# Optimization experiments

Hardware: AMD Instinct MI355X
Metric: run time of the kernel (lower is better)

The kernel has to match this reference:

```python
import jax, jax.numpy as jnp
import numpy as np

N0 = 260000  # all sampled nodes (hop-2 sources)
N1 = 60000   # hop-1 targets / hop-2 sources
N2 = 10000   # final batch targets
E1 = 1500000
E2 = 250000
DIN, DH, DOUT = 128, 256, 128


def sage_conv(x_src, x_tgt, src, dst, n_tgt, Wl, b, Wr):
    # mean aggregation of source features over incoming edges per target,
    # then lin_l(agg) + lin_r(x_tgt)  (PyG SAGEConv default, lin_r has no bias)
    msg = x_src[src]                                             # [E, d]
    agg = jax.ops.segment_sum(msg, dst, num_segments=n_tgt)      # [n_tgt, d]
    cnt = jax.ops.segment_sum(jnp.ones((src.shape[0], 1), x_src.dtype), dst,
                              num_segments=n_tgt)                # [n_tgt, 1]
    agg = agg / jnp.maximum(cnt, 1.0)
    return agg @ Wl + b + x_tgt @ Wr


def setup_inputs() -> dict:
    key = jax.random.key(0)
    ks = jax.random.split(key, 10)
    s = 1.0 / np.sqrt(DIN)
    s2 = 1.0 / np.sqrt(DH)
    return {
        "x": jax.random.normal(ks[0], (N0, DIN), dtype=jnp.float32),
        "W1l": jax.random.normal(ks[1], (DIN, DH), dtype=jnp.float32) * s,
        "b1": jnp.zeros((DH,), dtype=jnp.float32),
        "W1r": jax.random.normal(ks[2], (DIN, DH), dtype=jnp.float32) * s,
        "W2l": jax.random.normal(ks[3], (DH, DOUT), dtype=jnp.float32) * s2,
        "b2": jnp.zeros((DOUT,), dtype=jnp.float32),
        "W2r": jax.random.normal(ks[4], (DH, DOUT), dtype=jnp.float32) * s2,
        "src1": jax.random.randint(ks[5], (E1,), 0, N0, dtype=jnp.int32),
        "dst1": jax.random.randint(ks[6], (E1,), 0, N1, dtype=jnp.int32),
        "src2": jax.random.randint(ks[7], (E2,), 0, N1, dtype=jnp.int32),
        "dst2": jax.random.randint(ks[8], (E2,), 0, N2, dtype=jnp.int32),
    }


def reference(x, W1l, b1, W1r, W2l, b2, W2r, src1, dst1, src2, dst2):
    h = sage_conv(x, x[:N1], src1, dst1, N1, W1l, b1, W1r)  # [N1, DH]
    h = jax.nn.relu(h)
    out = sage_conv(h, h[:N2], src2, dst2, N2, W2l, b2, W2r)  # [N2, DOUT]
    return out
```

## Files before the change

kernel.cpp:

```cpp
#include <hip/hip_runtime.h>
#include <hip/hip_bf16.h>

#define N0 260000
#define N1 60000
#define N2 10000
#define E1 1500000
#define E2 250000
#define DIN 128
#define DH 256
#define DOUT 128
#define CAP 80

typedef __attribute__((ext_vector_type(8))) short bf16x8;
typedef __attribute__((ext_vector_type(4))) float f32x4;
typedef __attribute__((ext_vector_type(2))) float f32x2;
typedef __attribute__((ext_vector_type(4))) unsigned uivec4;

#define MFMA16(a, b, c) __builtin_amdgcn_mfma_f32_16x16x32_bf16(a, b, c, 0, 0, 0)

__device__ inline float blo(unsigned u) { return __uint_as_float(u << 16); }
__device__ inline float bhi(unsigned u) { return __uint_as_float(u & 0xFFFF0000u); }
__device__ inline unsigned short f2b(float f) {
    unsigned u = __float_as_uint(f);
    return (unsigned short)((u + 0x7FFFu + ((u >> 16) & 1u)) >> 16);
}

__device__ inline unsigned pack4_fp8(float4 f) {
    int w = 0;
    w = __builtin_amdgcn_cvt_pk_fp8_f32(f.x, f.y, w, false);
    w = __builtin_amdgcn_cvt_pk_fp8_f32(f.z, f.w, w, true);
    return (unsigned)w;
}
__device__ inline void acc8h(float* acc, uint2 v) {
    f32x2 a0 = __builtin_amdgcn_cvt_pk_f32_fp8((int)v.x, false);
    f32x2 a1 = __builtin_amdgcn_cvt_pk_f32_fp8((int)v.x, true);
    f32x2 a2 = __builtin_amdgcn_cvt_pk_f32_fp8((int)v.y, false);
    f32x2 a3 = __builtin_amdgcn_cvt_pk_f32_fp8((int)v.y, true);
    acc[0] += a0.x; acc[1] += a0.y; acc[2] += a1.x; acc[3] += a1.y;
    acc[4] += a2.x; acc[5] += a2.y; acc[6] += a3.x; acc[7] += a3.y;
}

#define BB_C1 256
#define BB_C2 64
#define BUILD2_BLOCKS (8 * BB_C2)
#define P1ROWS (N1 / 8)
#define P2ROWS (N2 / 8)
#define CONVX_BLOCKS 8125
#define CONVW_BLOCKS 512
#define CONV_TOTAL (CONVX_BLOCKS + CONVW_BLOCKS)
#define PERIOD 40
#define NPERIODS 256
#define INTERLEAVED (PERIOD * NPERIODS)
#define PREP_TAIL (CONV_TOTAL - 32 * NPERIODS)
#define PREP_BLOCKS (INTERLEAVED + PREP_TAIL)
__global__ __launch_bounds__(256) void prep9(const float* __restrict__ x, unsigned char* __restrict__ xb,
                                             const float* __restrict__ W1l, const float* __restrict__ W1r,
                                             const float* __restrict__ W2l, const float* __restrict__ W2r,
                                             unsigned short* __restrict__ W1lt, unsigned short* __restrict__ W1rt,
                                             unsigned short* __restrict__ W2lt, unsigned short* __restrict__ W2rt,
                                             const int* __restrict__ src1, const int* __restrict__ dst1,
                                             int* __restrict__ cnt1, int* __restrict__ csr1,
                                             int use_xb) {
    int b = blockIdx.x;
    int t = threadIdx.x;
    int conv_idx;
    if (b < INTERLEAVED) {
        int p = b / PERIOD, r = b % PERIOD;
        if (r < 8) {
            if (b == 0 && t < 16 && use_xb) {
                uint2 z; z.x = 0u; z.y = 0u;
                reinterpret_cast<uint2*>(xb + (size_t)N0 * DIN)[t] = z;
            }
            int lo = r * P1ROWS, hi = lo + P1ROWS;
            const int4* d4 = reinterpret_cast<const int4*>(dst1);
            const int4* s4 = reinterpret_cast<const int4*>(src1);
            for (int i = p * 256 + t; i < E1 / 4; i += BB_C1 * 256) {
                int4 d = d4[i];
                int4 s = s4[i];
                if (d.x >= lo && d.x < hi) { int q = atomicAdd(&cnt1[d.x], 1); if (q < CAP) csr1[d.x * CAP + q] = s.x; }
                if (d.y >= lo && d.y < hi) { int q = atomicAdd(&cnt1[d.y], 1); if (q < CAP) csr1[d.y * CAP + q] = s.y; }
                if (d.z >= lo && d.z < hi) { int q = atomicAdd(&cnt1[d.z], 1); if (q < CAP) csr1[d.z * CAP + q] = s.z; }
                if (d.w >= lo && d.w < hi) { int q = atomicAdd(&cnt1[d.w], 1); if (q < CAP) csr1[d.w * CAP + q] = s.w; }
            }
            return;
        }
        conv_idx = p * 32 + (r - 8);
    } else {
        conv_idx = 32 * NPERIODS + (b - INTERLEAVED);
    }
    if (conv_idx < CONVX_BLOCKS) {
        if (!use_xb) return;
        size_t i = (size_t)conv_idx * 256 + t;
        const float4* xf = reinterpret_cast<const float4*>(x) + i * 4;
        float4 f0 = xf[0], f1 = xf[1], f2 = xf[2], f3 = xf[3];
        uivec4 w;
        w.x = pack4_fp8(f0);
        w.y = pack4_fp8(f1);
        w.z = pack4_fp8(f2);
        w.w = pack4_fp8(f3);
        __builtin_nontemporal_store(w, reinterpret_cast<uivec4*>(xb + i * 16));
    } else {
        int tid = (conv_idx - CONVX_BLOCKS) * 256 + t;
        int seg = tid >> 15, idx = tid & 32767;
        if (seg == 0)      { int n = idx >> 7, k = idx & 127; W1lt[idx] = f2b(W1l[k * DH + n]); }
        else if (seg == 1) { int n = idx >> 7, k = idx & 127; W1rt[idx] = f2b(W1r[k * DH + n]); }
        else if (seg == 2) { int n = idx >> 8, k = idx & 255; W2lt[idx] = f2b(W2l[k * DOUT + n]); }
        else               { int n = idx >> 8, k = idx & 255; W2rt[idx] = f2b(W2r[k * DOUT + n]); }
    }
}

template <int XB>
__global__ __launch_bounds__(256) void agg_gemm1_k(const float* __restrict__ xf,
                                                   const unsigned char* __restrict__ xb,
                                                   const int* __restrict__ cnt,
                                                   const int* __restrict__ csr,
                                                   const unsigned short* __restrict__ Wlt,
                                                   const unsigned short* __restrict__ Wrt,
                                                   const float* __restrict__ b1,
                                                   unsigned short* __restrict__ hb,
                                                   const int* __restrict__ src2, const int* __restrict__ dst2,
                                                   int* __restrict__ cnt2, int* __restrict__ csr2) {
    __shared__ __align__(16) unsigned short lds[4352];
    const int XT0 = 2176;
    int t = threadIdx.x;
    if (blockIdx.x < BUILD2_BLOCKS) {
        int bb = blockIdx.x;
        if (bb == 0 && t < 64) {
            uint2 z; z.x = 0u; z.y = 0u;
            reinterpret_cast<uint2*>(hb + (size_t)N1 * DH)[t] = z;
        }
        int part = bb & 7, q = bb >> 3;
        int lo = part * P2ROWS, hi = lo + P2ROWS;
        const int4* d4 = reinterpret_cast<const int4*>(dst2);
        const int4* s4 = reinterpret_cast<const int4*>(src2);
        for (int i = q * 256 + t; i < E2 / 4; i += BB_C2 * 256) {
            int4 d = d4[i];
            int4 s = s4[i];
            if (d.x >= lo && d.x < hi) { int p = atomicAdd(&cnt2[d.x], 1); if (p < CAP) csr2[d.x * CAP + p] = s.x; }
            if (d.y >= lo && d.y < hi) { int p = atomicAdd(&cnt2[d.y], 1); if (p < CAP) csr2[d.y * CAP + p] = s.y; }
            if (d.z >= lo && d.z < hi) { int p = atomicAdd(&cnt2[d.z], 1); if (p < CAP) csr2[d.z * CAP + p] = s.z; }
            if (d.w >= lo && d.w < hi) { int p = atomicAdd(&cnt2[d.w], 1); if (p < CAP) csr2[d.w * CAP + p] = s.w; }
        }
        return;
    }
    int row0 = (blockIdx.x - BUILD2_BLOCKS) * 16;
    int r = t >> 4, li = t & 15;
    int rawc = cnt[row0 + r];
    int deg = rawc > CAP ? CAP : rawc;
    int beg = (row0 + r) * CAP, end = beg + deg;
    float acc[8];
#pragma unroll
    for (int j = 0; j < 8; ++j) acc[j] = 0.0f;
    {
        const float4* xf4 = reinterpret_cast<const float4*>(xf);
        float4 x0 = xf4[(size_t)(row0 + r) * 32 + li * 2];
        float4 x1 = xf4[(size_t)(row0 + r) * 32 + li * 2 + 1];
        bf16x8 xv;
        xv[0] = (short)f2b(x0.x); xv[1] = (short)f2b(x0.y); xv[2] = (short)f2b(x0.z); xv[3] = (short)f2b(x0.w);
        xv[4] = (short)f2b(x1.x); xv[5] = (short)f2b(x1.y); xv[6] = (short)f2b(x1.z); xv[7] = (short)f2b(x1.w);
        *reinterpret_cast<bf16x8*>(&lds[XT0 + r * 136 + li * 8]) = xv;
    }
    if (XB) {
        const uint2* base = reinterpret_cast<const uint2*>(xb);
        int nbatch = (deg + 7) >> 3;
        if (nbatch > 0) {
            int e0 = beg;
            int4 ra = *reinterpret_cast<const int4*>(csr + e0);
            int4 rb = *reinterpret_cast<const int4*>(csr + e0 + 4);
            for (int bb = 0; bb + 1 < nbatch; ++bb) {
                int4 na  = *reinterpret_cast<const int4*>(csr + e0 + 8);
                int4 nb4 = *reinterpret_cast<const int4*>(csr + e0 + 12);
                uint2 v0 = base[(size_t)ra.x * 16 + li];
                uint2 v1 = base[(size_t)ra.y * 16 + li];
                uint2 v2 = base[(size_t)ra.z * 16 + li];
                uint2 v3 = base[(size_t)ra.w * 16 + li];
                uint2 v4 = base[(size_t)rb.x * 16 + li];
                uint2 v5 = base[(size_t)rb.y * 16 + li];
                uint2 v6 = base[(size_t)rb.z * 16 + li];
                uint2 v7 = base[(size_t)rb.w * 16 + li];
                acc8h(acc, v0); acc8h(acc, v1); acc8h(acc, v2); acc8h(acc, v3);
                acc8h(acc, v4); acc8h(acc, v5); acc8h(acc, v6); acc8h(acc, v7);
                ra = na; rb = nb4; e0 += 8;
            }
            int s0 = (e0 + 0 < end) ? ra.x : N0;
            int s1 = (e0 + 1 < end) ? ra.y : N0;
            int s2 = (e0 + 2 < end) ? ra.z : N0;
            int s3 = (e0 + 3 < end) ? ra.w : N0;
            int s4i = (e0 + 4 < end) ? rb.x : N0;
            int s5 = (e0 + 5 < end) ? rb.y : N0;
            int s6 = (e0 + 6 < end) ? rb.z : N0;
            int s7 = (e0 + 7 < end) ? rb.w : N0;
            uint2 v0 = base[(size_t)s0 * 16 + li];
            uint2 v1 = base[(size_t)s1 * 16 + li];
            uint2 v2 = base[(size_t)s2 * 16 + li];
            uint2 v3 = base[(size_t)s3 * 16 + li];
            uint2 v4 = base[(size_t)s4i * 16 + li];
            uint2 v5 = base[(size_t)s5 * 16 + li];
            uint2 v6 = base[(size_t)s6 * 16 + li];
            uint2 v7 = base[(size_t)s7 * 16 + li];
            acc8h(acc, v0); acc8h(acc, v1); acc8h(acc, v2); acc8h(acc, v3);
            acc8h(acc, v4); acc8h(acc, v5); acc8h(acc, v6); acc8h(acc, v7);
        }
    } else {
        const float4* xf4 = reinterpret_cast<const float4*>(xf);
        for (int e = beg; e < end; ++e) {
            int s = csr[e];
            float4 v0 = xf4[(size_t)s * 32 + li * 2];
            float4 v1 = xf4[(size_t)s * 32 + li * 2 + 1];
            acc[0] += v0.x; acc[1] += v0.y; acc[2] += v0.z; acc[3] += v0.w;
            acc[4] += v1.x; acc[5] += v1.y; acc[6] += v1.z; acc[7] += v1.w;
        }
    }
    float inv = 1.0f / fmaxf((float)rawc, 1.0f);
    bf16x8 av;
#pragma unroll
    for (int j = 0; j < 8; ++j) av[j] = (short)f2b(acc[j] * inv);
    *reinterpret_cast<bf16x8*>(&lds[r * 136 + li * 8]) = av;
    __syncthreads();

    int l = t & 63, w = t >> 6;
    f32x4 c[4];
#pragma unroll
    for (int nt = 0; nt < 4; ++nt) c[nt] = (f32x4){0.f, 0.f, 0.f, 0.f};
    int arow = (l & 15) * 136;
    int colbase = w * 64 + (l & 15);
    int kbase = (l >> 4) * 8;
#pragma unroll
    for (int kk = 0; kk < 4; ++kk) {
        int goff = arow + (kk * 4 + (l >> 4)) * 8;
        bf16x8 af = *reinterpret_cast<const bf16x8*>(&lds[goff]);
        bf16x8 tf = *reinterpret_cast<const bf16x8*>(&lds[XT0 + goff]);
        int k = kk * 32 + kbase;
#pragma unroll
        for (int nt = 0; nt < 4; ++nt) {
            int n = colbase + nt * 16;
            bf16x8 wl = *reinterpret_cast<const bf16x8*>(&Wlt[n * DIN + k]);
            bf16x8 wr = *reinterpret_cast<const bf16x8*>(&Wrt[n * DIN + k]);
            c[nt] = MFMA16(af, wl, c[nt]);
            c[nt] = MFMA16(tf, wr, c[nt]);
        }
    }
    __syncthreads();
#pragma unroll
    for (int nt = 0; nt < 4; ++nt) {
        int col = colbase + nt * 16;
        float bias = b1[col];
#pragma unroll
        for (int j = 0; j < 4; ++j) {
            int rr = (l >> 4) * 4 + j;
            lds[rr * 264 + col] = f2b(fmaxf(c[nt][j] + bias, 0.0f));
        }
    }
    __syncthreads();
#pragma unroll
    for (int i = 0; i < 2; ++i) {
        int gi = t + i * 256;
        int rr = gi >> 5, g = gi & 31;
        *reinterpret_cast<uint4*>(&hb[(size_t)(row0 + rr) * 256 + g * 8]) =
            *reinterpret_cast<const uint4*>(&lds[rr * 264 + g * 8]);
    }
}

__global__ __launch_bounds__(512) void agg_gemm2_k(const unsigned short* __restrict__ hb,
                                                   const int* __restrict__ cnt,
                                                   const int* __restrict__ csr,
                                                   const unsigned short* __restrict__ Wlt,
                                                   const unsigned short* __restrict__ Wrt,
                                                   const float* __restrict__ b2,
                                                   float* __restrict__ out) {
    __shared__ __align__(16) unsigned short lds[8448];
    const int HT0 = 4224;
    int t = threadIdx.x;
    int row0 = blockIdx.x * 16;
    int r = t >> 5, li = t & 31;
    int rawc = cnt[row0 + r];
    int deg = rawc > CAP ? CAP : rawc;
    int beg = (row0 + r) * CAP, end = beg + deg;
    float acc[8];
#pragma unroll
    for (int j = 0; j < 8; ++j) acc[j] = 0.0f;
    const uint4* base = reinterpret_cast<const uint4*>(hb);
    *reinterpret_cast<uint4*>(&lds[HT0 + r * 264 + li * 8]) =
        reinterpret_cast<const uint4*>(&hb[(size_t)(row0 + r) * 256])[li];
    int nbatch = (deg + 7) >> 3;
    if (nbatch > 0) {
        int e0 = beg;
        int4 ra = *reinterpret_cast<const int4*>(csr + e0);
        int4 rb = *reinterpret_cast<const int4*>(csr + e0 + 4);
        for (int bb = 0; bb + 1 < nbatch; ++bb) {
            int4 na  = *reinterpret_cast<const int4*>(csr + e0 + 8);
            int4 nb4 = *reinterpret_cast<const int4*>(csr + e0 + 12);
            uint4 v0 = base[(size_t)ra.x * 32 + li];
            uint4 v1 = base[(size_t)ra.y * 32 + li];
            uint4 v2 = base[(size_t)ra.z * 32 + li];
            uint4 v3 = base[(size_t)ra.w * 32 + li];
            uint4 v4 = base[(size_t)rb.x * 32 + li];
            uint4 v5 = base[(size_t)rb.y * 32 + li];
            uint4 v6 = base[(size_t)rb.z * 32 + li];
            uint4 v7 = base[(size_t)rb.w * 32 + li];
            acc[0] += blo(v0.x) + blo(v1.x) + blo(v2.x) + blo(v3.x) + blo(v4.x) + blo(v5.x) + blo(v6.x) + blo(v7.x);
            acc[1] += bhi(v0.x) + bhi(v1.x) + bhi(v2.x) + bhi(v3.x) + bhi(v4.x) + bhi(v5.x) + bhi(v6.x) + bhi(v7.x);
            acc[2] += blo(v0.y) + blo(v1.y) + blo(v2.y) + blo(v3.y) + blo(v4.y) + blo(v5.y) + blo(v6.y) + blo(v7.y);
            acc[3] += bhi(v0.y) + bhi(v1.y) + bhi(v2.y) + bhi(v3.y) + bhi(v4.y) + bhi(v5.y) + bhi(v6.y) + bhi(v7.y);
            acc[4] += blo(v0.z) + blo(v1.z) + blo(v2.z) + blo(v3.z) + blo(v4.z) + blo(v5.z) + blo(v6.z) + blo(v7.z);
            acc[5] += bhi(v0.z) + bhi(v1.z) + bhi(v2.z) + bhi(v3.z) + bhi(v4.z) + bhi(v5.z) + bhi(v6.z) + bhi(v7.z);
            acc[6] += blo(v0.w) + blo(v1.w) + blo(v2.w) + blo(v3.w) + blo(v4.w) + blo(v5.w) + blo(v6.w) + blo(v7.w);
            acc[7] += bhi(v0.w) + bhi(v1.w) + bhi(v2.w) + bhi(v3.w) + bhi(v4.w) + bhi(v5.w) + bhi(v6.w) + bhi(v7.w);
            ra = na; rb = nb4; e0 += 8;
        }
        int s0 = (e0 + 0 < end) ? ra.x : N1;
        int s1 = (e0 + 1 < end) ? ra.y : N1;
        int s2 = (e0 + 2 < end) ? ra.z : N1;
        int s3 = (e0 + 3 < end) ? ra.w : N1;
        int s4i = (e0 + 4 < end) ? rb.x : N1;
        int s5 = (e0 + 5 < end) ? rb.y : N1;
        int s6 = (e0 + 6 < end) ? rb.z : N1;
        int s7 = (e0 + 7 < end) ? rb.w : N1;
        uint4 v0 = base[(size_t)s0 * 32 + li];
        uint4 v1 = base[(size_t)s1 * 32 + li];
        uint4 v2 = base[(size_t)s2 * 32 + li];
        uint4 v3 = base[(size_t)s3 * 32 + li];
        uint4 v4 = base[(size_t)s4i * 32 + li];
        uint4 v5 = base[(size_t)s5 * 32 + li];
        uint4 v6 = base[(size_t)s6 * 32 + li];
        uint4 v7 = base[(size_t)s7 * 32 + li];
        acc[0] += blo(v0.x) + blo(v1.x) + blo(v2.x) + blo(v3.x) + blo(v4.x) + blo(v5.x) + blo(v6.x) + blo(v7.x);
        acc[1] += bhi(v0.x) + bhi(v1.x) + bhi(v2.x) + bhi(v3.x) + bhi(v4.x) + bhi(v5.x) + bhi(v6.x) + bhi(v7.x);
        acc[2] += blo(v0.y) + blo(v1.y) + blo(v2.y) + blo(v3.y) + blo(v4.y) + blo(v5.y) + blo(v6.y) + blo(v7.y);
        acc[3] += bhi(v0.y) + bhi(v1.y) + bhi(v2.y) + bhi(v3.y) + bhi(v4.y) + bhi(v5.y) + bhi(v6.y) + bhi(v7.y);
        acc[4] += blo(v0.z) + blo(v1.z) + blo(v2.z) + blo(v3.z) + blo(v4.z) + blo(v5.z) + blo(v6.z) + blo(v7.z);
        acc[5] += bhi(v0.z) + bhi(v1.z) + bhi(v2.z) + bhi(v3.z) + bhi(v4.z) + bhi(v5.z) + bhi(v6.z) + bhi(v7.z);
        acc[6] += blo(v0.w) + blo(v1.w) + blo(v2.w) + blo(v3.w) + blo(v4.w) + blo(v5.w) + blo(v6.w) + blo(v7.w);
        acc[7] += bhi(v0.w) + bhi(v1.w) + bhi(v2.w) + bhi(v3.w) + bhi(v4.w) + bhi(v5.w) + bhi(v6.w) + bhi(v7.w);
    }
    float inv = 1.0f / fmaxf((float)rawc, 1.0f);
    bf16x8 av;
#pragma unroll
    for (int j = 0; j < 8; ++j) av[j] = (short)f2b(acc[j] * inv);
    *reinterpret_cast<bf16x8*>(&lds[r * 264 + li * 8]) = av;
    __syncthreads();

    int l = t & 63, w = t >> 6;
    f32x4 c = (f32x4){0.f, 0.f, 0.f, 0.f};
    int arow = (l & 15) * 264;
    int col = w * 16 + (l & 15);
    int kbase = (l >> 4) * 8;
#pragma unroll
    for (int kk = 0; kk < 8; ++kk) {
        int goff = arow + (kk * 4 + (l >> 4)) * 8;
        bf16x8 af = *reinterpret_cast<const bf16x8*>(&lds[goff]);
        bf16x8 hf = *reinterpret_cast<const bf16x8*>(&lds[HT0 + goff]);
        int k = kk * 32 + kbase;
        bf16x8 wl = *reinterpret_cast<const bf16x8*>(&Wlt[col * DH + k]);
        bf16x8 wr = *reinterpret_cast<const bf16x8*>(&Wrt[col * DH + k]);
        c = MFMA16(af, wl, c);
        c = MFMA16(hf, wr, c);
    }
    __syncthreads();
    float* O = reinterpret_cast<float*>(lds);
    float bias = b2[col];
#pragma unroll
    for (int j = 0; j < 4; ++j) {
        int rr = (l >> 4) * 4 + j;
        O[rr * 132 + col] = c[j] + bias;
    }
    __syncthreads();
    {
        int rr = t >> 5, c4 = t & 31;
        reinterpret_cast<float4*>(&out[(size_t)(row0 + rr) * 128])[c4] =
            reinterpret_cast<const float4*>(O)[rr * 33 + c4];
    }
}

extern "C" void kernel_launch(void* const* d_in, const int* in_sizes, int n_in,
                              void* d_out, int out_size, void* d_ws, size_t ws_size,
                              hipStream_t stream) {
    const float* x   = (const float*)d_in[0];
    const float* W1l = (const float*)d_in[1];
    const float* b1  = (const float*)d_in[2];
    const float* W1r = (const float*)d_in[3];
    const float* W2l = (const float*)d_in[4];
    const float* b2  = (const float*)d_in[5];
    const float* W2r = (const float*)d_in[6];
    const int* src1  = (const int*)d_in[7];
    const int* dst1  = (const int*)d_in[8];
    const int* src2  = (const int*)d_in[9];
    const int* dst2  = (const int*)d_in[10];
    float* out = (float*)d_out;

    char* ws = (char*)d_ws;
    size_t off = 0;
    auto alloc = [&](size_t bytes) { void* p = ws + off; off += (bytes + 255) & ~(size_t)255; return p; };
    int* cnt1    = (int*)alloc((size_t)N1 * 4);
    int* cnt2    = (int*)alloc((size_t)N2 * 4);
    int* csr1    = (int*)alloc((size_t)N1 * CAP * 4);
    int* csr2    = (int*)alloc((size_t)N2 * CAP * 4);
    unsigned short* W1lt = (unsigned short*)alloc((size_t)DIN * DH * 2);
    unsigned short* W1rt = (unsigned short*)alloc((size_t)DIN * DH * 2);
    unsigned short* W2lt = (unsigned short*)alloc((size_t)DH * DOUT * 2);
    unsigned short* W2rt = (unsigned short*)alloc((size_t)DH * DOUT * 2);
    unsigned short* hb   = (unsigned short*)alloc((size_t)(N1 + 1) * DH * 2);
    unsigned char* xb    = (unsigned char*)alloc((size_t)(N0 + 1) * DIN);
    int use_xb = (off <= ws_size) ? 1 : 0;

    hipMemsetAsync(cnt1, 0, (size_t)((char*)cnt2 - (char*)cnt1) + (size_t)N2 * 4, stream);

    prep9<<<PREP_BLOCKS, 256, 0, stream>>>(
        x, xb, W1l, W1r, W2l, W2r, W1lt, W1rt, W2lt, W2rt,
        src1, dst1, cnt1, csr1, use_xb);

    if (use_xb)
        agg_gemm1_k<1><<<BUILD2_BLOCKS + N1 / 16, 256, 0, stream>>>(x, xb, cnt1, csr1, W1lt, W1rt, b1, hb,
                                                                    src2, dst2, cnt2, csr2);
    else
        agg_gemm1_k<0><<<BUILD2_BLOCKS + N1 / 16, 256, 0, stream>>>(x, nullptr, cnt1, csr1, W1lt, W1rt, b1, hb,
                                                                    src2, dst2, cnt2, csr2);

    agg_gemm2_k<<<N2 / 16, 512, 0, stream>>>(hb, cnt2, csr2, W2lt, W2rt, b2, out);
}
```

Before: 215.4 us.

## Split layer-1 neighbor aggregation across two half-warps per row with 512-thread blocks

Doubles agg_gemm1 block size to 512 threads so each target row gets 32 lanes. The two 16-lane halves gather alternating 8-edge batches and combine their partial sums through shared memory. The GEMM stage is split so each wave computes 32 output columns instead of 64. This raises memory-level parallelism for the gather, which is latency bound. In exchange it drops the software prefetch of CSR indices, adds an extra barrier and LDS traffic, and uses a larger LDS footprint per block.

Measured after the change: 219.8 us. 2.0% more time.

```diff
diff --git a/kernel.cpp b/kernel.cpp
--- a/kernel.cpp
+++ b/kernel.cpp
@@ -110,7 +110,7 @@
 }
 
 template <int XB>
-__global__ __launch_bounds__(256) void agg_gemm1_k(const float* __restrict__ xf,
+__global__ __launch_bounds__(512) void agg_gemm1_k(const float* __restrict__ xf,
                                                    const unsigned char* __restrict__ xb,
                                                    const int* __restrict__ cnt,
                                                    const int* __restrict__ csr,
@@ -120,8 +120,9 @@
                                                    unsigned short* __restrict__ hb,
                                                    const int* __restrict__ src2, const int* __restrict__ dst2,
                                                    int* __restrict__ cnt2, int* __restrict__ csr2) {
-    __shared__ __align__(16) unsigned short lds[4352];
+    __shared__ __align__(16) unsigned short lds[8960];
     const int XT0 = 2176;
+    float* part = reinterpret_cast<float*>(&lds[4352]);
     int t = threadIdx.x;
     if (blockIdx.x < BUILD2_BLOCKS) {
         int bb = blockIdx.x;
@@ -129,11 +130,11 @@
             uint2 z; z.x = 0u; z.y = 0u;
             reinterpret_cast<uint2*>(hb + (size_t)N1 * DH)[t] = z;
         }
-        int part = bb & 7, q = bb >> 3;
-        int lo = part * P2ROWS, hi = lo + P2ROWS;
+        int part_id = bb & 7, q = bb >> 3;
+        int lo = part_id * P2ROWS, hi = lo + P2ROWS;
         const int4* d4 = reinterpret_cast<const int4*>(dst2);
         const int4* s4 = reinterpret_cast<const int4*>(src2);
-        for (int i = q * 256 + t; i < E2 / 4; i += BB_C2 * 256) {
+        for (int i = q * 512 + t; i < E2 / 4; i += BB_C2 * 512) {
             int4 d = d4[i];
             int4 s = s4[i];
             if (d.x >= lo && d.x < hi) { int p = atomicAdd(&cnt2[d.x], 1); if (p < CAP) csr2[d.x * CAP + p] = s.x; }
@@ -144,14 +145,17 @@
         return;
     }
     int row0 = (blockIdx.x - BUILD2_BLOCKS) * 16;
-    int r = t >> 4, li = t & 15;
+    int r = t >> 5;
+    int li32 = t & 31;
+    int half = li32 >> 4;
+    int li = li32 & 15;
     int rawc = cnt[row0 + r];
     int deg = rawc > CAP ? CAP : rawc;
     int beg = (row0 + r) * CAP, end = beg + deg;
     float acc[8];
 #pragma unroll
     for (int j = 0; j < 8; ++j) acc[j] = 0.0f;
-    {
+    if (half == 0) {
         const float4* xf4 = reinterpret_cast<const float4*>(xf);
         float4 x0 = xf4[(size_t)(row0 + r) * 32 + li * 2];
         float4 x1 = xf4[(size_t)(row0 + r) * 32 + li * 2 + 1];
@@ -162,26 +166,9 @@
     }
     if (XB) {
         const uint2* base = reinterpret_cast<const uint2*>(xb);
-        int nbatch = (deg + 7) >> 3;
-        if (nbatch > 0) {
-            int e0 = beg;
+        for (int e0 = beg + half * 8; e0 < end; e0 += 16) {
             int4 ra = *reinterpret_cast<const int4*>(csr + e0);
             int4 rb = *reinterpret_cast<const int4*>(csr + e0 + 4);
-            for (int bb = 0; bb + 1 < nbatch; ++bb) {
-                int4 na  = *reinterpret_cast<const int4*>(csr + e0 + 8);
-                int4 nb4 = *reinterpret_cast<const int4*>(csr + e0 + 12);
-                uint2 v0 = base[(size_t)ra.x * 16 + li];
-                uint2 v1 = base[(size_t)ra.y * 16 + li];
-                uint2 v2 = base[(size_t)ra.z * 16 + li];
-                uint2 v3 = base[(size_t)ra.w * 16 + li];
-                uint2 v4 = base[(size_t)rb.x * 16 + li];
-                uint2 v5 = base[(size_t)rb.y * 16 + li];
-                uint2 v6 = base[(size_t)rb.z * 16 + li];
-                uint2 v7 = base[(size_t)rb.w * 16 + li];
-                acc8h(acc, v0); acc8h(acc, v1); acc8h(acc, v2); acc8h(acc, v3);
-                acc8h(acc, v4); acc8h(acc, v5); acc8h(acc, v6); acc8h(acc, v7);
-                ra = na; rb = nb4; e0 += 8;
-            }
             int s0 = (e0 + 0 < end) ? ra.x : N0;
             int s1 = (e0 + 1 < end) ? ra.y : N0;
             int s2 = (e0 + 2 < end) ? ra.z : N0;
@@ -203,7 +190,7 @@
         }
     } else {
         const float4* xf4 = reinterpret_cast<const float4*>(xf);
-        for (int e = beg; e < end; ++e) {
+        for (int e = beg + half; e < end; e += 2) {
             int s = csr[e];
             float4 v0 = xf4[(size_t)s * 32 + li * 2];
             float4 v1 = xf4[(size_t)s * 32 + li * 2 + 1];
@@ -211,19 +198,26 @@
             acc[4] += v1.x; acc[5] += v1.y; acc[6] += v1.z; acc[7] += v1.w;
         }
     }
-    float inv = 1.0f / fmaxf((float)rawc, 1.0f);
-    bf16x8 av;
-#pragma unroll
-    for (int j = 0; j < 8; ++j) av[j] = (short)f2b(acc[j] * inv);
-    *reinterpret_cast<bf16x8*>(&lds[r * 136 + li * 8]) = av;
+    if (half == 1) {
+#pragma unroll
+        for (int j = 0; j < 8; ++j) part[(r * 16 + li) * 9 + j] = acc[j];
+    }
+    __syncthreads();
+    if (half == 0) {
+        float inv = 1.0f / fmaxf((float)rawc, 1.0f);
+        bf16x8 av;
+#pragma unroll
+        for (int j = 0; j < 8; ++j) av[j] = (short)f2b((acc[j] + part[(r * 16 + li) * 9 + j]) * inv);
+        *reinterpret_cast<bf16x8*>(&lds[r * 136 + li * 8]) = av;
+    }
     __syncthreads();
 
     int l = t & 63, w = t >> 6;
-    f32x4 c[4];
-#pragma unroll
-    for (int nt = 0; nt < 4; ++nt) c[nt] = (f32x4){0.f, 0.f, 0.f, 0.f};
+    f32x4 c[2];
+    c[0] = (f32x4){0.f, 0.f, 0.f, 0.f};
+    c[1] = (f32x4){0.f, 0.f, 0.f, 0.f};
     int arow = (l & 15) * 136;
-    int colbase = w * 64 + (l & 15);
+    int colbase = w * 32 + (l & 15);
     int kbase = (l >> 4) * 8;
 #pragma unroll
     for (int kk = 0; kk < 4; ++kk) {
@@ -232,7 +226,7 @@
         bf16x8 tf = *reinterpret_cast<const bf16x8*>(&lds[XT0 + goff]);
         int k = kk * 32 + kbase;
 #pragma unroll
-        for (int nt = 0; nt < 4; ++nt) {
+        for (int nt = 0; nt < 2; ++nt) {
             int n = colbase + nt * 16;
             bf16x8 wl = *reinterpret_cast<const bf16x8*>(&Wlt[n * DIN + k]);
             bf16x8 wr = *reinterpret_cast<const bf16x8*>(&Wrt[n * DIN + k]);
@@ -242,7 +236,7 @@
     }
     __syncthreads();
 #pragma unroll
-    for (int nt = 0; nt < 4; ++nt) {
+    for (int nt = 0; nt < 2; ++nt) {
         int col = colbase + nt * 16;
         float bias = b1[col];
 #pragma unroll
@@ -252,10 +246,8 @@
         }
     }
     __syncthreads();
-#pragma unroll
-    for (int i = 0; i < 2; ++i) {
-        int gi = t + i * 256;
-        int rr = gi >> 5, g = gi & 31;
+    {
+        int rr = t >> 5, g = t & 31;
         *reinterpret_cast<uint4*>(&hb[(size_t)(row0 + rr) * 256 + g * 8]) =
             *reinterpret_cast<const uint4*>(&lds[rr * 264 + g * 8]);
     }
@@ -410,10 +402,10 @@
         src1, dst1, cnt1, csr1, use_xb);
 
     if (use_xb)
-        agg_gemm1_k<1><<<BUILD2_BLOCKS + N1 / 16, 256, 0, stream>>>(x, xb, cnt1, csr1, W1lt, W1rt, b1, hb,
+        agg_gemm1_k<1><<<BUILD2_BLOCKS + N1 / 16, 512, 0, stream>>>(x, xb, cnt1, csr1, W1lt, W1rt, b1, hb,
                                                                     src2, dst2, cnt2, csr2);
     else
-        agg_gemm1_k<0><<<BUILD2_BLOCKS + N1 / 16, 256, 0, stream>>>(x, nullptr, cnt1, csr1, W1lt, W1rt, b1, hb,
+        agg_gemm1_k<0><<<BUILD2_BLOCKS + N1 / 16, 512, 0, stream>>>(x, nullptr, cnt1, csr1, W1lt, W1rt, b1, hb,
                                                                     src2, dst2, cnt2, csr2);
 
     agg_gemm2_k<<<N2 / 16, 512, 0, stream>>>(hb, cnt2, csr2, W2lt, W2rt, b2, out);
```
